# Kernel tuning notes

Measured on AMD Instinct MI355X. Metric: run time of the kernel, lower is better.

## Reference

```python
import jax, jax.numpy as jnp
import numpy as np

# S5 layer: ZOH discretization of diagonal complex SSM + parallel associative scan
# u: (B, L, H) real; state dim P (complex diagonal Lambda)

DT_MIN, DT_MAX = 1e-3, 1e-1
STEP_RESCALE = 1.0

def setup_inputs() -> dict:
    key = jax.random.key(0)
    ks = jax.random.split(key, 7)
    Bsz, L, H, P = 8, 4096, 1024, 512
    u = jax.random.normal(ks[0], (Bsz, L, H), jnp.float32)
    # HiPPO-like diagonal: negative real part, spread imaginary part
    Lambda_re = -0.5 * jnp.abs(jax.random.normal(ks[1], (P,), jnp.float32)) - 0.1
    Lambda_im = jnp.pi * jax.random.normal(ks[2], (P,), jnp.float32)
    # B: (P, H, 2) real/imag stacked (xavier-ish scale); C: (H, P, 2)
    Bp = jax.random.normal(ks[3], (P, H, 2), jnp.float32) / np.sqrt(H)
    Cp = jax.random.normal(ks[4], (H, P, 2), jnp.float32) / np.sqrt(P)
    D = jax.random.normal(ks[5], (H,), jnp.float32)
    log_step = jnp.log(jax.random.uniform(ks[6], (P, 1), jnp.float32) * (DT_MAX - DT_MIN) + DT_MIN)
    return {"u": u, "Lambda_re": Lambda_re, "Lambda_im": Lambda_im,
            "B": Bp, "C": Cp, "D": D, "log_step": log_step}


def _s5_forward(u, Lambda_re, Lambda_im, B, C, D, log_step):
    # clip_eigs=True: keep real part strictly negative
    Lambda = jnp.minimum(Lambda_re, -1e-4) + 1j * Lambda_im          # (P,)
    B_tilde = (B[..., 0] + 1j * B[..., 1]).astype(jnp.complex64)      # (P, H)
    C_tilde = (C[..., 0] + 1j * C[..., 1]).astype(jnp.complex64)      # (H, P)
    step = STEP_RESCALE * jnp.exp(log_step[:, 0])                     # (P,)
    # ZOH discretization
    Lambda_bar = jnp.exp(Lambda * step)                               # (P,)
    B_bar = ((Lambda_bar - 1.0) / Lambda)[:, None] * B_tilde          # (P, H)
    # input projection into state space
    Bu = jnp.einsum('blh,ph->blp', u.astype(jnp.complex64), B_bar)    # (B, L, P)
    A = jnp.broadcast_to(Lambda_bar, Bu.shape)                        # (B, L, P)
    # linear recurrence x_k = Lambda_bar * x_{k-1} + Bu_k via log-depth scan
    def combine(e_i, e_j):
        a_i, b_i = e_i
        a_j, b_j = e_j
        return a_j * a_i, a_j * b_i + b_j
    _, xs = jax.lax.associative_scan(combine, (A, Bu), axis=1)        # (B, L, P)
    # readout
    ys = jnp.einsum('blp,hp->blh', xs, C_tilde).real + D * u          # (B, L, H)
    return ys


def reference(u, Lambda_re, Lambda_im, B, C, D, log_step):
    return _s5_forward(u, Lambda_re, Lambda_im, B, C, D, log_step)
```

## Files before the change

### kernel.cpp

```cpp
#include <hip/hip_runtime.h>


#define Bsz 8
#define Lseq 4096
#define Hdim 1024
#define Pdim 512
#define NCHUNK 64
#define CHUNK 64
#define MROWS 32768

typedef __attribute__((ext_vector_type(8))) __bf16 bf16x8;
typedef __attribute__((ext_vector_type(4))) float f32x4;

__device__ __forceinline__ unsigned short f2bf(float f) {
  union { float f; unsigned u; } v; v.f = f;
  unsigned r = v.u + 0x7fffu + ((v.u >> 16) & 1u);
  return (unsigned short)(r >> 16);
}
__device__ __forceinline__ float bf2f(unsigned short s) {
  union { unsigned u; float f; } v; v.u = ((unsigned)s) << 16;
  return v.f;
}

__device__ __forceinline__ void gld_lds16(const void* g, void* l) {
  __builtin_amdgcn_global_load_lds(
      (const __attribute__((address_space(1))) unsigned int*)g,
      (__attribute__((address_space(3))) unsigned int*)l, 16, 0, 0);
}

__global__ void k_setup(const float* __restrict__ Lre_in, const float* __restrict__ Lim_in,
                        const float* __restrict__ log_step,
                        float2* __restrict__ a_arr, float2* __restrict__ aS_arr,
                        float2* __restrict__ g_arr) {
  int p = threadIdx.x;
  if (p >= Pdim) return;
  float lre = fminf(Lre_in[p], -1e-4f);
  float lim = Lim_in[p];
  float step = expf(log_step[p]);
  float zr = lre * step, zi = lim * step;
  float er = expf(zr);
  float ar = er * cosf(zi), ai = er * sinf(zi);
  a_arr[p] = make_float2(ar, ai);
  float erS = expf(zr * (float)CHUNK);
  aS_arr[p] = make_float2(erS * cosf(zi * (float)CHUNK), erS * sinf(zi * (float)CHUNK));
  float den = lre * lre + lim * lim;
  float nr = ar - 1.0f, ni = ai;
  g_arr[p] = make_float2((nr * lre + ni * lim) / den, (ni * lre - nr * lim) / den);
}

__global__ void k_prep_B(const float* __restrict__ Bin, const float2* __restrict__ g_arr,
                         unsigned short* __restrict__ Bbar2) {
  int idx = blockIdx.x * 256 + threadIdx.x;
  int p = idx >> 10;
  int h = idx & 1023;
  float B0 = Bin[2 * idx];
  float B1 = Bin[2 * idx + 1];
  float2 g = g_arr[p];
  Bbar2[(size_t)p * Hdim + h]            = f2bf(g.x * B0 - g.y * B1);
  Bbar2[(size_t)(Pdim + p) * Hdim + h]   = f2bf(g.x * B1 + g.y * B0);
}

__global__ void k_prep_C(const float* __restrict__ Cin, unsigned short* __restrict__ C2m) {
  int idx = blockIdx.x * 256 + threadIdx.x;
  int h = idx >> 9;
  int p = idx & 511;
  float C0 = Cin[2 * idx];
  float C1 = Cin[2 * idx + 1];
  C2m[(size_t)h * 1024 + p]        = f2bf(C0);
  C2m[(size_t)h * 1024 + 512 + p]  = f2bf(-C1);
}

__global__ void k_cvt_u(const float* __restrict__ u, unsigned short* __restrict__ ub) {
  size_t i = ((size_t)blockIdx.x * 256 + threadIdx.x) * 4;
  float4 v = *(const float4*)(u + i);
  ushort4 o;
  o.x = f2bf(v.x); o.y = f2bf(v.y); o.z = f2bf(v.z); o.w = f2bf(v.w);
  *(ushort4*)(ub + i) = o;
}

template <int EPI>
__global__ __launch_bounds__(256, 4) void gemm_bt(const unsigned short* __restrict__ A,
                                                  const unsigned short* __restrict__ Bt,
                                                  void* __restrict__ Cout,
                                                  const float* __restrict__ uin,
                                                  const float* __restrict__ Dvec) {
  const int K = 1024;
  __shared__ __align__(16) unsigned short sm[16384];
  char* smc = (char*)sm;

  int tid = threadIdx.x;
  int lane = tid & 63;
  int w = tid >> 6;
  int wr = w >> 1, wc = w & 1;
  int quad = lane >> 4;
  int mrow = lane & 15;

  size_t rowBase = (size_t)blockIdx.x * 128;
  size_t colBase = (size_t)blockIdx.y * 128;

  f32x4 acc[4][4];
#pragma unroll
  for (int i = 0; i < 4; i++)
#pragma unroll
    for (int j = 0; j < 4; j++) acc[i][j] = (f32x4){0.f, 0.f, 0.f, 0.f};

  int r0 = tid >> 2;
  int cst = (tid & 3) ^ ((tid >> 3) & 3);
  const unsigned short* pa0 = A + rowBase * K + (size_t)r0 * K + cst * 8;
  const unsigned short* pa1 = pa0 + (size_t)64 * K;
  const unsigned short* pb0 = Bt + colBase * K + (size_t)r0 * K + cst * 8;
  const unsigned short* pb1 = pb0 + (size_t)64 * K;
  int dA0 = w * 1024, dA1 = 4096 + w * 1024;
  int dB0 = 8192 + w * 1024, dB1 = 12288 + w * 1024;

  int cr = quad ^ ((mrow >> 1) & 3);
  int aOff = (wr * 64 + mrow) * 32 + cr * 8;
  int bOff = 4096 + (wc * 64 + mrow) * 32 + cr * 8;

  gld_lds16(pa0, smc + dA0);
  gld_lds16(pa1, smc + dA1);
  gld_lds16(pb0, smc + dB0);
  gld_lds16(pb1, smc + dB1);

  for (int i = 0; i < 32; ++i) {
    __syncthreads();
    int cur = i & 1;
    if (i < 31) {
      int kb = (i + 1) * 32;
      int bb = (cur ^ 1) * 16384;
      gld_lds16(pa0 + kb, smc + bb + dA0);
      gld_lds16(pa1 + kb, smc + bb + dA1);
      gld_lds16(pb0 + kb, smc + bb + dB0);
      gld_lds16(pb1 + kb, smc + bb + dB1);
    }
    const unsigned short* Ab = sm + cur * 8192 + aOff;
    const unsigned short* Bb = sm + cur * 8192 + bOff;
    bf16x8 af[4], bfv[4];
#pragma unroll
    for (int mt = 0; mt < 4; mt++) af[mt] = *(const bf16x8*)(Ab + mt * 512);
#pragma unroll
    for (int nt = 0; nt < 4; nt++) bfv[nt] = *(const bf16x8*)(Bb + nt * 512);
#pragma unroll
    for (int mt = 0; mt < 4; mt++)
#pragma unroll
      for (int nt = 0; nt < 4; nt++)
        acc[mt][nt] = __builtin_amdgcn_mfma_f32_16x16x32_bf16(af[mt], bfv[nt], acc[mt][nt], 0, 0, 0);
  }

  if (EPI == 0) {
    unsigned short* O = (unsigned short*)Cout;
    __syncthreads();
#pragma unroll
    for (int ph = 0; ph < 2; ph++) {
      if (wr == ph) {
#pragma unroll
        for (int mt = 0; mt < 4; mt++)
#pragma unroll
          for (int nt = 0; nt < 4; nt++)
#pragma unroll
            for (int r = 0; r < 4; r++) {
              int lr = mt * 16 + quad * 4 + r;
              int col = wc * 64 + nt * 16 + mrow;
              sm[lr * 136 + col] = f2bf(acc[mt][nt][r]);
            }
      }
      __syncthreads();
#pragma unroll
      for (int it = 0; it < 4; it++) {
        int cid = it * 256 + tid;
        int lr = cid >> 4;
        int cc = cid & 15;
        uint4 v = *(const uint4*)(sm + lr * 136 + cc * 8);
        *(uint4*)(O + (rowBase + ph * 64 + lr) * 1024 + colBase + cc * 8) = v;
      }
      __syncthreads();
    }
  } else {
    float* O = (float*)Cout;
    size_t mBase = rowBase + wr * 64 + quad * 4;
    size_t nBase = colBase + wc * 64 + mrow;
#pragma unroll
    for (int mt = 0; mt < 4; mt++)
#pragma unroll
      for (int nt = 0; nt < 4; nt++) {
        size_t n = nBase + nt * 16;
        float dv = Dvec[n];
#pragma unroll
        for (int r = 0; r < 4; r++) {
          size_t m = mBase + mt * 16 + r;
          O[m * 1024 + n] = acc[mt][nt][r] + dv * uin[m * 1024 + n];
        }
      }
  }
}

__global__ void k_scan1(const unsigned short* __restrict__ Bu, const float2* __restrict__ a_arr,
                        float* __restrict__ carryT) {
  int bc = blockIdx.x;
  int p = blockIdx.y * 256 + threadIdx.x;
  int b = bc >> 6, c = bc & 63;
  float2 a = a_arr[p];
  const unsigned short* bu = Bu + ((size_t)b * Lseq + (size_t)c * CHUNK) * 1024;
  float tr = 0.f, ti = 0.f;
#pragma unroll 8
  for (int l = 0; l < CHUNK; l++) {
    float br = bf2f(bu[(size_t)l * 1024 + p]);
    float bi = bf2f(bu[(size_t)l * 1024 + 512 + p]);
    float nr = fmaf(a.x, tr, fmaf(-a.y, ti, br));
    ti = fmaf(a.x, ti, fmaf(a.y, tr, bi));
    tr = nr;
  }
  carryT[(size_t)bc * 1024 + p] = tr;
  carryT[(size_t)bc * 1024 + 512 + p] = ti;
}

__global__ void k_scan2(const float* __restrict__ carryT, const float2* __restrict__ aS_arr,
                        float* __restrict__ prefix) {
  int b = blockIdx.x;
  int p = blockIdx.y * 256 + threadIdx.x;
  float2 s = aS_arr[p];
  float xr = 0.f, xi = 0.f;
#pragma unroll
  for (int c = 0; c < NCHUNK; c++) {
    size_t o = ((size_t)(b * NCHUNK + c)) * 1024 + p;
    prefix[o] = xr;
    prefix[o + 512] = xi;
    float tr = carryT[o], ti = carryT[o + 512];
    float nr = fmaf(s.x, xr, fmaf(-s.y, xi, tr));
    xi = fmaf(s.x, xi, fmaf(s.y, xr, ti));
    xr = nr;
  }
}

__global__ void k_scan3(const unsigned short* __restrict__ Bu, const float2* __restrict__ a_arr,
                        const float* __restrict__ prefix, unsigned short* __restrict__ xs) {
  int bc = blockIdx.x;
  int p = blockIdx.y * 256 + threadIdx.x;
  int b = bc >> 6, c = bc & 63;
  float2 a = a_arr[p];
  size_t base = ((size_t)b * Lseq + (size_t)c * CHUNK) * 1024;
  size_t po = (size_t)bc * 1024 + p;
  float xr = prefix[po], xi = prefix[po + 512];
#pragma unroll 8
  for (int l = 0; l < CHUNK; l++) {
    float br = bf2f(Bu[base + (size_t)l * 1024 + p]);
    float bi = bf2f(Bu[base + (size_t)l * 1024 + 512 + p]);
    float nr = fmaf(a.x, xr, fmaf(-a.y, xi, br));
    xi = fmaf(a.x, xi, fmaf(a.y, xr, bi));
    xr = nr;
    xs[base + (size_t)l * 1024 + p] = f2bf(xr);
    xs[base + (size_t)l * 1024 + 512 + p] = f2bf(xi);
  }
}

extern "C" void kernel_launch(void* const* d_in, const int* in_sizes, int n_in,
                              void* d_out, int out_size, void* d_ws, size_t ws_size,
                              hipStream_t stream) {
  const float* u     = (const float*)d_in[0];
  const float* Lre   = (const float*)d_in[1];
  const float* Lim   = (const float*)d_in[2];
  const float* Bin   = (const float*)d_in[3];
  const float* Cin   = (const float*)d_in[4];
  const float* Dvec  = (const float*)d_in[5];
  const float* lstep = (const float*)d_in[6];

  char* ws = (char*)d_ws;
  unsigned short* ubf_xs = (unsigned short*)(ws);
  unsigned short* Bbar2  = (unsigned short*)(ws + 67108864);
  unsigned short* C2m    = (unsigned short*)(ws + 69206016);
  float*          carryT = (float*)(ws + 71303168);
  float*          prefix = (float*)(ws + 73400320);
  float2*         a_arr  = (float2*)(ws + 75497472);
  float2*         aS_arr = (float2*)(ws + 75501568);
  float2*         g_arr  = (float2*)(ws + 75505664);

  unsigned short* Bu = (unsigned short*)d_out;

  k_setup<<<1, 512, 0, stream>>>(Lre, Lim, lstep, a_arr, aS_arr, g_arr);
  k_prep_B<<<2048, 256, 0, stream>>>(Bin, g_arr, Bbar2);
  k_prep_C<<<2048, 256, 0, stream>>>(Cin, C2m);
  k_cvt_u<<<32768, 256, 0, stream>>>(u, ubf_xs);

  gemm_bt<0><<<dim3(256, 8), 256, 0, stream>>>(ubf_xs, Bbar2, (void*)Bu, nullptr, nullptr);

  k_scan1<<<dim3(Bsz * NCHUNK, 2), 256, 0, stream>>>(Bu, a_arr, carryT);
  k_scan2<<<dim3(Bsz, 2), 256, 0, stream>>>(carryT, aS_arr, prefix);
  k_scan3<<<dim3(Bsz * NCHUNK, 2), 256, 0, stream>>>(Bu, a_arr, prefix, ubf_xs);

  gemm_bt<1><<<dim3(256, 8), 256, 0, stream>>>(ubf_xs, C2m, d_out, u, Dvec);
}
```

Before: 498.0 us.

## Parallelize chunk-carry scan with wave shuffles and vectorize scan loads

The sequential 64-step carry propagation in k_scan2 becomes a wavefront-parallel Hillis-Steele scan using __shfl_up, with one wave per (batch, state) pair, so the serial loop over chunks is removed. k_scan1 and k_scan3 now handle two state elements per thread with 32-bit packed bf16 loads and stores, which halves the number of memory instructions. The GEMM grid is flattened to 1D with column-fastest block ordering so neighbouring blocks share A rows in cache, and the launch-bounds occupancy hint goes from 4 to 5. The higher occupancy target may force register spills in the GEMM.

Measured after the change: 496.8 us. No clear change (-0.2%).

```diff
diff --git a/kernel.cpp b/kernel.cpp
--- a/kernel.cpp
+++ b/kernel.cpp
@@ -79,7 +79,7 @@
 }
 
 template <int EPI>
-__global__ __launch_bounds__(256, 4) void gemm_bt(const unsigned short* __restrict__ A,
+__global__ __launch_bounds__(256, 5) void gemm_bt(const unsigned short* __restrict__ A,
                                                   const unsigned short* __restrict__ Bt,
                                                   void* __restrict__ Cout,
                                                   const float* __restrict__ uin,
@@ -95,8 +95,9 @@
   int quad = lane >> 4;
   int mrow = lane & 15;
 
-  size_t rowBase = (size_t)blockIdx.x * 128;
-  size_t colBase = (size_t)blockIdx.y * 128;
+  int wg = blockIdx.x;
+  size_t rowBase = (size_t)(wg >> 3) * 128;
+  size_t colBase = (size_t)(wg & 7) * 128;
 
   f32x4 acc[4][4];
 #pragma unroll
@@ -197,59 +198,84 @@
 __global__ void k_scan1(const unsigned short* __restrict__ Bu, const float2* __restrict__ a_arr,
                         float* __restrict__ carryT) {
   int bc = blockIdx.x;
-  int p = blockIdx.y * 256 + threadIdx.x;
+  int p0 = threadIdx.x * 2;
   int b = bc >> 6, c = bc & 63;
-  float2 a = a_arr[p];
+  float2 a0 = a_arr[p0], a1 = a_arr[p0 + 1];
   const unsigned short* bu = Bu + ((size_t)b * Lseq + (size_t)c * CHUNK) * 1024;
-  float tr = 0.f, ti = 0.f;
+  float tr0 = 0.f, ti0 = 0.f, tr1 = 0.f, ti1 = 0.f;
 #pragma unroll 8
   for (int l = 0; l < CHUNK; l++) {
-    float br = bf2f(bu[(size_t)l * 1024 + p]);
-    float bi = bf2f(bu[(size_t)l * 1024 + 512 + p]);
-    float nr = fmaf(a.x, tr, fmaf(-a.y, ti, br));
-    ti = fmaf(a.x, ti, fmaf(a.y, tr, bi));
-    tr = nr;
-  }
-  carryT[(size_t)bc * 1024 + p] = tr;
-  carryT[(size_t)bc * 1024 + 512 + p] = ti;
+    unsigned vr = *(const unsigned*)(bu + (size_t)l * 1024 + p0);
+    unsigned vi = *(const unsigned*)(bu + (size_t)l * 1024 + 512 + p0);
+    float br0 = bf2f((unsigned short)vr), br1 = bf2f((unsigned short)(vr >> 16));
+    float bi0 = bf2f((unsigned short)vi), bi1 = bf2f((unsigned short)(vi >> 16));
+    float nr0 = fmaf(a0.x, tr0, fmaf(-a0.y, ti0, br0));
+    ti0 = fmaf(a0.x, ti0, fmaf(a0.y, tr0, bi0));
+    tr0 = nr0;
+    float nr1 = fmaf(a1.x, tr1, fmaf(-a1.y, ti1, br1));
+    ti1 = fmaf(a1.x, ti1, fmaf(a1.y, tr1, bi1));
+    tr1 = nr1;
+  }
+  *(float2*)(carryT + (size_t)bc * 1024 + p0) = make_float2(tr0, tr1);
+  *(float2*)(carryT + (size_t)bc * 1024 + 512 + p0) = make_float2(ti0, ti1);
 }
 
 __global__ void k_scan2(const float* __restrict__ carryT, const float2* __restrict__ aS_arr,
                         float* __restrict__ prefix) {
-  int b = blockIdx.x;
-  int p = blockIdx.y * 256 + threadIdx.x;
+  int wid = blockIdx.x * 4 + (threadIdx.x >> 6);
+  int lane = threadIdx.x & 63;
+  int b = wid >> 9;
+  int p = wid & 511;
   float2 s = aS_arr[p];
-  float xr = 0.f, xi = 0.f;
-#pragma unroll
-  for (int c = 0; c < NCHUNK; c++) {
-    size_t o = ((size_t)(b * NCHUNK + c)) * 1024 + p;
-    prefix[o] = xr;
-    prefix[o + 512] = xi;
-    float tr = carryT[o], ti = carryT[o + 512];
-    float nr = fmaf(s.x, xr, fmaf(-s.y, xi, tr));
-    xi = fmaf(s.x, xi, fmaf(s.y, xr, ti));
-    xr = nr;
-  }
+  size_t o = ((size_t)(b * NCHUNK + lane)) * 1024 + p;
+  float tr = carryT[o], ti = carryT[o + 512];
+  float mr = s.x, mi = s.y;
+#pragma unroll
+  for (int d = 1; d < 64; d <<= 1) {
+    float ur = __shfl_up(tr, d, 64);
+    float ui = __shfl_up(ti, d, 64);
+    if (lane >= d) {
+      tr = fmaf(mr, ur, fmaf(-mi, ui, tr));
+      ti = fmaf(mr, ui, fmaf(mi, ur, ti));
+    }
+    float nmr = mr * mr - mi * mi;
+    mi = 2.f * mr * mi;
+    mr = nmr;
+  }
+  float er = __shfl_up(tr, 1, 64);
+  float ei = __shfl_up(ti, 1, 64);
+  if (lane == 0) { er = 0.f; ei = 0.f; }
+  prefix[o] = er;
+  prefix[o + 512] = ei;
 }
 
 __global__ void k_scan3(const unsigned short* __restrict__ Bu, const float2* __restrict__ a_arr,
                         const float* __restrict__ prefix, unsigned short* __restrict__ xs) {
   int bc = blockIdx.x;
-  int p = blockIdx.y * 256 + threadIdx.x;
+  int p0 = threadIdx.x * 2;
   int b = bc >> 6, c = bc & 63;
-  float2 a = a_arr[p];
+  float2 a0 = a_arr[p0], a1 = a_arr[p0 + 1];
   size_t base = ((size_t)b * Lseq + (size_t)c * CHUNK) * 1024;
-  size_t po = (size_t)bc * 1024 + p;
-  float xr = prefix[po], xi = prefix[po + 512];
+  size_t po = (size_t)bc * 1024 + p0;
+  float2 xrv = *(const float2*)(prefix + po);
+  float2 xiv = *(const float2*)(prefix + po + 512);
+  float xr0 = xrv.x, xr1 = xrv.y, xi0 = xiv.x, xi1 = xiv.y;
 #pragma unroll 8
   for (int l = 0; l < CHUNK; l++) {
-    float br = bf2f(Bu[base + (size_t)l * 1024 + p]);
-    float bi = bf2f(Bu[base + (size_t)l * 1024 + 512 + p]);
-    float nr = fmaf(a.x, xr, fmaf(-a.y, xi, br));
-    xi = fmaf(a.x, xi, fmaf(a.y, xr, bi));
-    xr = nr;
-    xs[base + (size_t)l * 1024 + p] = f2bf(xr);
-    xs[base + (size_t)l * 1024 + 512 + p] = f2bf(xi);
+    unsigned vr = *(const unsigned*)(Bu + base + (size_t)l * 1024 + p0);
+    unsigned vi = *(const unsigned*)(Bu + base + (size_t)l * 1024 + 512 + p0);
+    float br0 = bf2f((unsigned short)vr), br1 = bf2f((unsigned short)(vr >> 16));
+    float bi0 = bf2f((unsigned short)vi), bi1 = bf2f((unsigned short)(vi >> 16));
+    float nr0 = fmaf(a0.x, xr0, fmaf(-a0.y, xi0, br0));
+    xi0 = fmaf(a0.x, xi0, fmaf(a0.y, xr0, bi0));
+    xr0 = nr0;
+    float nr1 = fmaf(a1.x, xr1, fmaf(-a1.y, xi1, br1));
+    xi1 = fmaf(a1.x, xi1, fmaf(a1.y, xr1, bi1));
+    xr1 = nr1;
+    unsigned orv = (unsigned)f2bf(xr0) | ((unsigned)f2bf(xr1) << 16);
+    unsigned oiv = (unsigned)f2bf(xi0) | ((unsigned)f2bf(xi1) << 16);
+    *(unsigned*)(xs + base + (size_t)l * 1024 + p0) = orv;
+    *(unsigned*)(xs + base + (size_t)l * 1024 + 512 + p0) = oiv;
   }
 }
 
@@ -281,11 +307,11 @@
   k_prep_C<<<2048, 256, 0, stream>>>(Cin, C2m);
   k_cvt_u<<<32768, 256, 0, stream>>>(u, ubf_xs);
 
-  gemm_bt<0><<<dim3(256, 8), 256, 0, stream>>>(ubf_xs, Bbar2, (void*)Bu, nullptr, nullptr);
-
-  k_scan1<<<dim3(Bsz * NCHUNK, 2), 256, 0, stream>>>(Bu, a_arr, carryT);
-  k_scan2<<<dim3(Bsz, 2), 256, 0, stream>>>(carryT, aS_arr, prefix);
-  k_scan3<<<dim3(Bsz * NCHUNK, 2), 256, 0, stream>>>(Bu, a_arr, prefix, ubf_xs);
-
-  gemm_bt<1><<<dim3(256, 8), 256, 0, stream>>>(ubf_xs, C2m, d_out, u, Dvec);
-}
+  gemm_bt<0><<<2048, 256, 0, stream>>>(ubf_xs, Bbar2, (void*)Bu, nullptr, nullptr);
+
+  k_scan1<<<512, 256, 0, stream>>>(Bu, a_arr, carryT);
+  k_scan2<<<1024, 256, 0, stream>>>(carryT, aS_arr, prefix);
+  k_scan3<<<512, 256, 0, stream>>>(Bu, a_arr, prefix, ubf_xs);
+
+  gemm_bt<1><<<2048, 256, 0, stream>>>(ubf_xs, C2m, d_out, u, Dvec);
+}
```
